# Optimization experiments

Measured on AMD Instinct MI355X. Metric: run time of the kernel, lower is better.

## Reference

```python
import jax, jax.numpy as jnp
import numpy as np
from jax import lax


def _interp_matrix(n_in: int, n_out: int) -> jnp.ndarray:
    """Row-stochastic [n_out, n_in] matrix for 1-D linear interp, align_corners=True."""
    if n_in == 1:
        return jnp.ones((n_out, 1), dtype=jnp.float32)
    pos = jnp.arange(n_out, dtype=jnp.float32) * ((n_in - 1) / (n_out - 1))
    lo = jnp.clip(jnp.floor(pos).astype(jnp.int32), 0, n_in - 2)
    frac = pos - lo.astype(jnp.float32)
    rows = jnp.arange(n_out)
    W = jnp.zeros((n_out, n_in), dtype=jnp.float32)
    W = W.at[rows, lo].add(1.0 - frac)
    W = W.at[rows, lo + 1].add(frac)
    return W


def setup_inputs() -> dict:
    key = jax.random.key(0)
    ks = jax.random.split(key, 10)
    B, C, H, W = 8, 64, 128, 128
    Ch = C // 2
    x = jax.random.normal(ks[0], (B, C, H, W), dtype=jnp.float32)
    # fan-in scaled weights to keep softmax logits in a sane range
    pool_w = jax.random.normal(ks[1], (C, C, 3, 3), dtype=jnp.float32) / np.sqrt(C * 9)
    pool_b = jax.random.normal(ks[2], (C,), dtype=jnp.float32) * 0.1
    q_w = jax.random.normal(ks[3], (Ch, C), dtype=jnp.float32) / np.sqrt(C)
    q_b = jax.random.normal(ks[4], (Ch,), dtype=jnp.float32) * 0.1
    k_w = jax.random.normal(ks[5], (Ch, C), dtype=jnp.float32) / np.sqrt(C)
    k_b = jax.random.normal(ks[6], (Ch,), dtype=jnp.float32) * 0.1
    v_w = jax.random.normal(ks[7], (C, C), dtype=jnp.float32) / np.sqrt(C)
    v_b = jax.random.normal(ks[8], (C,), dtype=jnp.float32) * 0.1
    gamma = jax.random.normal(ks[9], (1,), dtype=jnp.float32)
    return {"x": x, "pool_w": pool_w, "pool_b": pool_b, "q_w": q_w, "q_b": q_b,
            "k_w": k_w, "k_b": k_b, "v_w": v_w, "v_b": v_b, "gamma": gamma}


def reference(x, pool_w, pool_b, q_w, q_b, k_w, k_b, v_w, v_b, gamma):
    # 3x3 stride-2 pad-1 conv (the 'pool')
    xp = lax.conv_general_dilated(x, pool_w, window_strides=(2, 2),
                                  padding=((1, 1), (1, 1)),
                                  dimension_numbers=('NCHW', 'OIHW', 'NCHW'))
    xp = xp + pool_b[None, :, None, None]
    B, C, h, w = xp.shape
    N = h * w
    xf = xp.reshape(B, C, N)  # [B, C, N]
    # 1x1 convs as matmuls over the channel dim
    q = jnp.einsum('oc,bcn->bon', q_w, xf) + q_b[None, :, None]   # [B, C/2, N]
    k = jnp.einsum('oc,bcn->bon', k_w, xf) + k_b[None, :, None]   # [B, C/2, N]
    v = jnp.einsum('oc,bcn->bon', v_w, xf) + v_b[None, :, None]   # [B, C, N]
    # energy[b, n, m] = <q[:, n], k[:, m]>  -> softmax over m
    energy = jnp.einsum('bdn,bdm->bnm', q, k)                     # [B, N, N]
    attn = jax.nn.softmax(energy, axis=-1)
    # out = value @ attention^T  (torch: bmm(v, attn.permute(0,2,1)))
    out = jnp.einsum('bcm,bnm->bcn', v, attn).reshape(B, C, h, w)
    out = gamma[0] * out
    # bilinear upsample to input size, align_corners=True (separable matmuls)
    H, Wd = x.shape[2], x.shape[3]
    Wh = _interp_matrix(h, H)
    Ww = _interp_matrix(w, Wd)
    out = jnp.einsum('Hh,bchw->bcHw', Wh, out)
    out = jnp.einsum('Ww,bchw->bchW', Ww, out)
    return out + x
```

## Files before the change

### kernel.cpp

```cpp
#include <hip/hip_runtime.h>


typedef __attribute__((ext_vector_type(8))) short bf16x8;
typedef __attribute__((ext_vector_type(4))) float f32x4;

#define DEV static __device__ __forceinline__

DEV unsigned f2bf(float f) {
  union { float f; unsigned u; } a; a.f = f;
  return (a.u + 0x7FFFu + ((a.u >> 16) & 1u)) >> 16;
}
DEV unsigned cvtpk(float lo, float hi) {
  unsigned r;
  asm("v_cvt_pk_bf16_f32 %0, %1, %2" : "=v"(r) : "v"(lo), "v"(hi));
  return r;
}
DEV bf16x8 mk_bf16x8(unsigned w0, unsigned w1, unsigned w2, unsigned w3) {
  union { unsigned u[4]; bf16x8 v; } x;
  x.u[0] = w0; x.u[1] = w1; x.u[2] = w2; x.u[3] = w3;
  return x.v;
}
DEV void gload_lds16(const void* g, void* l) {
  __builtin_amdgcn_global_load_lds(
      (const __attribute__((address_space(1))) void*)g,
      (__attribute__((address_space(3))) void*)l, 16, 0, 0);
}

__global__ __launch_bounds__(256) void prep_kernel(
    const float* __restrict__ pw, const float* __restrict__ qw,
    const float* __restrict__ kw, const float* __restrict__ vw,
    const float* __restrict__ qb, const float* __restrict__ kb,
    const float* __restrict__ vb,
    unsigned short* __restrict__ Ag, unsigned short* __restrict__ A2g,
    float* __restrict__ bias2) {
  const float LOG2E = 1.4426950408889634f;
  const int i = blockIdx.x * 256 + threadIdx.x;
  if (i < 36864) {
    const int oc = i / 576, k = i - oc * 576;
    const int tap = k >> 6, ic = k & 63;
    Ag[i] = (unsigned short)f2bf(pw[(oc * 64 + ic) * 9 + tap]);
  }
  const int j = i - 36864;
  if (j >= 0 && j < 8192) {
    const int r = j >> 6, c = j & 63;
    if (r < 32)       A2g[j] = (unsigned short)f2bf(qw[r * 64 + c] * LOG2E);
    else if (r < 64)  A2g[j] = (unsigned short)f2bf(kw[(r - 32) * 64 + c]);
    else              A2g[j] = (unsigned short)f2bf(vw[(r - 64) * 64 + c]);
  }
  if (j >= 8192 && j < 8320) {
    const int r = j - 8192;
    bias2[r] = r < 32 ? qb[r] * LOG2E : (r < 64 ? kb[r - 32] : vb[r - 64]);
  }
}

__global__ __launch_bounds__(256) void convqkv_kernel(
    const float* __restrict__ x, const unsigned short* __restrict__ Ag,
    const float* __restrict__ pool_b, const unsigned short* __restrict__ A2g,
    const float* __restrict__ bias2,
    unsigned short* __restrict__ qT, unsigned short* __restrict__ kT,
    unsigned short* __restrict__ vM) {
  const int b = blockIdx.x >> 6, oy = blockIdx.x & 63;
  const int t = threadIdx.x, w = t >> 6, lane = t & 63;
  const int lr = lane & 15, lg = lane >> 4;
  __shared__ unsigned short sIn[390 * 64];
  __shared__ unsigned short sXP[64 * 64];
  char* sInB = (char*)sIn;
  char* sXPB = (char*)sXP;

  bf16x8 af[18];
  {
    const unsigned short* ap = Ag + (w * 16 + lr) * 576 + (lg << 3);
    #pragma unroll
    for (int kc = 0; kc < 18; ++kc)
      af[kc] = *(const bf16x8*)(ap + kc * 32);
  }

  #pragma unroll
  for (int rr = 0; rr < 2; ++rr) {
    const int pos = t + rr * 256;
    if (pos < 390) {
      const int ky = pos / 130, xi = pos - ky * 130;
      const int iy = 2 * oy + ky - 1, ix = xi - 1;
      const bool ok = (iy >= 0) & (iy < 128) & (ix >= 0) & (ix < 128);
      const float* xs = x + ((size_t)(b * 64) * 128 + (ok ? iy : 0)) * 128 +
                        (ok ? ix : 0);
      const int sw = pos & 7;
      #pragma unroll
      for (int o = 0; o < 8; ++o) {
        float f[8];
        #pragma unroll
        for (int jj = 0; jj < 8; ++jj)
          f[jj] = ok ? xs[(size_t)(o * 8 + jj) * 16384] : 0.f;
        bf16x8 v = mk_bf16x8(cvtpk(f[0], f[1]), cvtpk(f[2], f[3]),
                             cvtpk(f[4], f[5]), cvtpk(f[6], f[7]));
        *(bf16x8*)(sInB + pos * 128 + ((o ^ sw) << 4)) = v;
      }
    }
  }
  __syncthreads();

  f32x4 acc[4];
  #pragma unroll
  for (int nt = 0; nt < 4; ++nt) acc[nt] = (f32x4){0.f, 0.f, 0.f, 0.f};
  #pragma unroll
  for (int kc = 0; kc < 18; ++kc) {
    const int tap = kc >> 1, ky = tap / 3, kx = tap - ky * 3;
    const int o = ((kc & 1) << 2) + lg;
    #pragma unroll
    for (int nt = 0; nt < 4; ++nt) {
      const int xi = 2 * (nt * 16 + lr) + kx;
      const int pos = ky * 130 + xi;
      bf16x8 bfr = *(const bf16x8*)(sInB + pos * 128 + ((o ^ (pos & 7)) << 4));
      acc[nt] = __builtin_amdgcn_mfma_f32_16x16x32_bf16(af[kc], bfr, acc[nt],
                                                        0, 0, 0);
    }
  }

  const int ocBase = w * 16 + (lg << 2);
  float pb[4];
  #pragma unroll
  for (int r = 0; r < 4; ++r) pb[r] = pool_b[ocBase + r];
  const int ocOct = ocBase >> 3;
  const int withinB = (ocBase & 7) * 2;
  #pragma unroll
  for (int nt = 0; nt < 4; ++nt) {
    const int pos = nt * 16 + lr;
    const unsigned p01 = cvtpk(acc[nt][0] + pb[0], acc[nt][1] + pb[1]);
    const unsigned p23 = cvtpk(acc[nt][2] + pb[2], acc[nt][3] + pb[3]);
    char* base = sXPB + pos * 128 + ((ocOct ^ (pos & 7)) << 4) + withinB;
    *(unsigned*)(base) = p01;
    *(unsigned*)(base + 4) = p23;
  }
  __syncthreads();

  bf16x8 a2[2][2];
  #pragma unroll
  for (int mt = 0; mt < 2; ++mt)
    #pragma unroll
    for (int kc2 = 0; kc2 < 2; ++kc2)
      a2[mt][kc2] = *(const bf16x8*)(A2g + ((2 * w + mt) * 16 + lr) * 64 +
                                     kc2 * 32 + (lg << 3));
  f32x4 acc2[2][4];
  #pragma unroll
  for (int mt = 0; mt < 2; ++mt)
    #pragma unroll
    for (int nt = 0; nt < 4; ++nt) acc2[mt][nt] = (f32x4){0.f, 0.f, 0.f, 0.f};
  #pragma unroll
  for (int kc2 = 0; kc2 < 2; ++kc2) {
    const int o2 = (kc2 << 2) + lg;
    #pragma unroll
    for (int nt = 0; nt < 4; ++nt) {
      const int pos = nt * 16 + lr;
      bf16x8 bfr = *(const bf16x8*)(sXPB + pos * 128 + ((o2 ^ (pos & 7)) << 4));
      acc2[0][nt] = __builtin_amdgcn_mfma_f32_16x16x32_bf16(a2[0][kc2], bfr,
                                                            acc2[0][nt], 0, 0, 0);
      acc2[1][nt] = __builtin_amdgcn_mfma_f32_16x16x32_bf16(a2[1][kc2], bfr,
                                                            acc2[1][nt], 0, 0, 0);
    }
  }

  const int n0g = oy << 6;
  #pragma unroll
  for (int mt = 0; mt < 2; ++mt) {
    const int rowB = (2 * w + mt) * 16 + (lg << 2);
    float b2[4];
    #pragma unroll
    for (int r = 0; r < 4; ++r) b2[r] = bias2[rowB + r];
    if (rowB < 32) {
      #pragma unroll
      for (int nt = 0; nt < 4; ++nt) {
        const int n = n0g + nt * 16 + lr;
        unsigned* dst = (unsigned*)(qT + (((size_t)(b << 12) + n) << 5) + rowB);
        dst[0] = cvtpk(acc2[mt][nt][0] + b2[0], acc2[mt][nt][1] + b2[1]);
        dst[1] = cvtpk(acc2[mt][nt][2] + b2[2], acc2[mt][nt][3] + b2[3]);
      }
    } else if (rowB < 64) {
      #pragma unroll
      for (int nt = 0; nt < 4; ++nt) {
        const int n = n0g + nt * 16 + lr;
        unsigned* dst = (unsigned*)(kT + (((size_t)(b << 12) + n) << 5) + rowB - 32);
        dst[0] = cvtpk(acc2[mt][nt][0] + b2[0], acc2[mt][nt][1] + b2[1]);
        dst[1] = cvtpk(acc2[mt][nt][2] + b2[2], acc2[mt][nt][3] + b2[3]);
      }
    } else {
      const int cv = rowB - 64;
      #pragma unroll
      for (int nt = 0; nt < 4; ++nt) {
        const int n = n0g + nt * 16 + lr;
        #pragma unroll
        for (int r = 0; r < 4; ++r)
          vM[(((size_t)(b << 6) + cv + r) << 12) + n] =
              (unsigned short)f2bf(acc2[mt][nt][r] + b2[r]);
      }
    }
  }
}

__global__ __launch_bounds__(256, 2) void attn_kernel(
    const unsigned short* __restrict__ qT, const unsigned short* __restrict__ kT,
    const unsigned short* __restrict__ vM,
    float* __restrict__ attnP, float* __restrict__ Lbuf) {
  __shared__ char lds[24576];
  __shared__ char Plds[4][4608];
  const int t = threadIdx.x, w = t >> 6, lane = t & 63;
  const int lr = lane & 15, lg = lane >> 4;
  const int b = blockIdx.x & 7;
  const int u = (blockIdx.x >> 3) & 31;
  const int split = blockIdx.x >> 8;
  const int n0 = (u << 7) + (w << 5);
  const int kb0 = split << 11;
  char* Pw = Plds[w];

  const unsigned short* qp = qT + (((size_t)(b << 12) + n0 + lr) << 5) + (lg << 3);
  const bf16x8 bq0 = *(const bf16x8*)(qp);
  const bf16x8 bq1 = *(const bf16x8*)(qp + (16 << 5));

  const unsigned short* ksrc = kT + ((size_t)(b << 12) << 5);
  const unsigned short* vsrc = vM + (((size_t)(b << 6) + lane) << 12);

  f32x4 acc[2][4];
  #pragma unroll
  for (int i = 0; i < 2; ++i)
    #pragma unroll
    for (int j = 0; j < 4; ++j) acc[i][j] = (f32x4){0.f, 0.f, 0.f, 0.f};
  float l_run[2] = {0.f, 0.f};

  #define STAGE(kb_, buf_) {                                                   \
    char* sb = lds + (buf_) * 12288;                                           \
    gload_lds16((const void*)(ksrc + (((size_t)(kb_) + lane) << 5) + (w << 3)),\
                sb + (w << 10));                                               \
    gload_lds16((const void*)(vsrc + (kb_) + (w << 4)),                        \
                sb + 4096 + (w << 11));                                        \
    gload_lds16((const void*)(vsrc + (kb_) + (w << 4) + 8),                    \
                sb + 4096 + (w << 11) + 1024);                                 \
  }

  STAGE(kb0, 0);
  __syncthreads();
  int buf = 0;

  for (int cc = 0; cc < 32; ++cc) {
    if (cc < 31) STAGE(kb0 + ((cc + 1) << 6), buf ^ 1);
    char* base = lds + buf * 12288;

    f32x4 st[2][4];
    const f32x4 z4 = {0.f, 0.f, 0.f, 0.f};
    __builtin_amdgcn_s_setprio(1);
    #pragma unroll
    for (int j = 0; j < 4; ++j) {
      const bf16x8 ka =
          *(const bf16x8*)(base + (((lg << 6) + (j << 4) + lr) << 4));
      st[0][j] = __builtin_amdgcn_mfma_f32_16x16x32_bf16(ka, bq0, z4, 0, 0, 0);
      st[1][j] = __builtin_amdgcn_mfma_f32_16x16x32_bf16(ka, bq1, z4, 0, 0, 0);
    }
    __builtin_amdgcn_s_setprio(0);

    #pragma unroll
    for (int nt = 0; nt < 2; ++nt) {
      float ps0 = 0.f, ps1 = 0.f;
      #pragma unroll
      for (int j = 0; j < 4; ++j) {
        const float p0 = __builtin_amdgcn_exp2f(st[nt][j][0]);
        const float p1 = __builtin_amdgcn_exp2f(st[nt][j][1]);
        const float p2 = __builtin_amdgcn_exp2f(st[nt][j][2]);
        const float p3 = __builtin_amdgcn_exp2f(st[nt][j][3]);
        ps0 += p0 + p1;
        ps1 += p2 + p3;
        *(uint2*)(Pw + (nt * 16 + lr) * 144 + (((j << 2) + lg) << 3)) =
            (uint2){cvtpk(p0, p1), cvtpk(p2, p3)};
      }
      l_run[nt] += ps0 + ps1;
    }

    #pragma unroll
    for (int h = 0; h < 2; ++h) {
      #pragma unroll
      for (int nt = 0; nt < 2; ++nt) {
        const bf16x8 pbf = *(const bf16x8*)(
            Pw + (nt * 16 + lr) * 144 + (((h << 3) + (lg << 1)) << 3));
        __builtin_amdgcn_s_setprio(1);
        #pragma unroll
        for (int ct = 0; ct < 4; ++ct) {
          const bf16x8 va = *(const bf16x8*)(
              base + 4096 + (((((h << 2) + lg) << 6) + (ct << 4) + lr) << 4));
          acc[nt][ct] = __builtin_amdgcn_mfma_f32_16x16x32_bf16(va, pbf,
                                                                acc[nt][ct], 0, 0, 0);
        }
        __builtin_amdgcn_s_setprio(0);
      }
    }
    __syncthreads();
    buf ^= 1;
  }

  #pragma unroll
  for (int nt = 0; nt < 2; ++nt) {
    l_run[nt] += __shfl_xor(l_run[nt], 16, 64);
    l_run[nt] += __shfl_xor(l_run[nt], 32, 64);
  }

  float* dstP = attnP + ((size_t)split << 21);
  #pragma unroll
  for (int nt = 0; nt < 2; ++nt) {
    const int q = n0 + (nt << 4) + lr;
    #pragma unroll
    for (int ct = 0; ct < 4; ++ct)
      #pragma unroll
      for (int r = 0; r < 4; ++r) {
        const int c = (ct << 4) + (lg << 2) + r;
        dstP[((size_t)((b << 6) + c) << 12) + q] = acc[nt][ct][r];
      }
  }
  if (lane < 16) {
    Lbuf[((size_t)(split * 8 + b) << 12) + n0 + lane] = l_run[0];
    Lbuf[((size_t)(split * 8 + b) << 12) + n0 + 16 + lane] = l_run[1];
  }
}

__global__ __launch_bounds__(256) void merge_kernel(
    float* __restrict__ attnP, const float* __restrict__ Lbuf,
    const float* __restrict__ gamma_p) {
  const int idx = blockIdx.x * 256 + threadIdx.x;
  const size_t base4 = (size_t)idx << 2;
  const int n4 = (int)(base4 & 4095);
  const int b = (int)(base4 >> 18);
  const f32x4 p0 = *(const f32x4*)(attnP + base4);
  const f32x4 p1 = *(const f32x4*)(attnP + (1u << 21) + base4);
  const f32x4 l0 = *(const f32x4*)(Lbuf + ((size_t)b << 12) + n4);
  const f32x4 l1 = *(const f32x4*)(Lbuf + ((size_t)(8 + b) << 12) + n4);
  const float g = gamma_p[0];
  f32x4 o;
  #pragma unroll
  for (int i = 0; i < 4; ++i) o[i] = (p0[i] + p1[i]) * g / (l0[i] + l1[i]);
  *(f32x4*)(attnP + base4) = o;
}

__global__ __launch_bounds__(256) void upsample_residual_kernel(
    const float* __restrict__ attn_out, const float* __restrict__ x,
    float* __restrict__ out) {
  const int idx = blockIdx.x * 256 + threadIdx.x;
  const int X0 = (idx & 31) << 2;
  int rem = idx >> 5;
  const int Y = rem & 127; rem >>= 7;
  const int c = rem & 63;
  const int b = rem >> 6;

  const float sr = 63.0f / 127.0f;
  float fy = Y * sr;
  int iy = (int)fy; if (iy > 62) iy = 62;
  const float ty = fy - (float)iy;
  const float* ap = attn_out + (((size_t)(b * 64 + c)) << 12);
  const float* r0 = ap + iy * 64;
  const float* r1 = r0 + 64;

  float tmp[4];
  #pragma unroll
  for (int k = 0; k < 4; ++k) {
    const int X = X0 + k;
    float fx = X * sr;
    int ix = (int)fx; if (ix > 62) ix = 62;
    const float tx = fx - (float)ix;
    float v0 = r0[ix] + tx * (r0[ix + 1] - r0[ix]);
    float v1 = r1[ix] + tx * (r1[ix + 1] - r1[ix]);
    tmp[k] = v0 + ty * (v1 - v0);
  }
  const size_t o = (((size_t)((b * 64 + c) * 128 + Y)) << 7) + X0;
  f32x4 xv = *reinterpret_cast<const f32x4*>(x + o);
  f32x4 ov = {tmp[0] + xv[0], tmp[1] + xv[1], tmp[2] + xv[2], tmp[3] + xv[3]};
  *reinterpret_cast<f32x4*>(out + o) = ov;
}

extern "C" void kernel_launch(void* const* d_in, const int* in_sizes, int n_in,
                              void* d_out, int out_size, void* d_ws, size_t ws_size,
                              hipStream_t stream) {
  const float* x      = (const float*)d_in[0];
  const float* pool_w = (const float*)d_in[1];
  const float* pool_b = (const float*)d_in[2];
  const float* q_w    = (const float*)d_in[3];
  const float* q_b    = (const float*)d_in[4];
  const float* k_w    = (const float*)d_in[5];
  const float* k_b    = (const float*)d_in[6];
  const float* v_w    = (const float*)d_in[7];
  const float* v_b    = (const float*)d_in[8];
  const float* gamma  = (const float*)d_in[9];
  float* out = (float*)d_out;

  char* ws = (char*)d_ws;
  unsigned short* Ag   = (unsigned short*)(ws);
  unsigned short* A2g  = (unsigned short*)(ws + 81920);
  float* bias2         = (float*)(ws + 98304);
  unsigned short* qT   = (unsigned short*)(ws + 1048576);
  unsigned short* kT   = (unsigned short*)(ws + 3145728);
  unsigned short* vM   = (unsigned short*)(ws + 5242880);
  float* attnP         = (float*)(ws + 9437184);
  float* Lbuf          = (float*)(ws + 26214400);

  prep_kernel<<<177, 256, 0, stream>>>(pool_w, q_w, k_w, v_w, q_b, k_b, v_b,
                                       Ag, A2g, bias2);
  convqkv_kernel<<<512, 256, 0, stream>>>(x, Ag, pool_b, A2g, bias2, qT, kT, vM);
  attn_kernel<<<512, 256, 0, stream>>>(qT, kT, vM, attnP, Lbuf);
  merge_kernel<<<2048, 256, 0, stream>>>(attnP, Lbuf, gamma);
  upsample_residual_kernel<<<8192, 256, 0, stream>>>(attnP, x, out);
}
```

Before: 93.46 us.

## Halve attention query tile per wave and transpose P via lane shuffles instead of LDS

Each wave now handles 16 queries instead of 32, doubling the grid to 1024 blocks and raising launch_bounds occupancy to 4 blocks per CU. The per-wave P staging buffer in LDS is removed; the exp'd probabilities are repacked into the MFMA B-operand layout with cross-lane shuffles. This aims to cut LDS use and round trips and to raise occupancy so latency is hidden better. In exchange, each K/V tile loaded into LDS is reused by half as many queries, which doubles global K/V traffic.

```diff
diff --git a/kernel.cpp b/kernel.cpp
--- a/kernel.cpp
+++ b/kernel.cpp
@@ -196,34 +196,33 @@
   }
 }
 
-__global__ __launch_bounds__(256, 2) void attn_kernel(
+__global__ __launch_bounds__(256, 4) void attn_kernel(
     const unsigned short* __restrict__ qT, const unsigned short* __restrict__ kT,
     const unsigned short* __restrict__ vM,
     float* __restrict__ attnP, float* __restrict__ Lbuf) {
   __shared__ char lds[24576];
-  __shared__ char Plds[4][4608];
   const int t = threadIdx.x, w = t >> 6, lane = t & 63;
   const int lr = lane & 15, lg = lane >> 4;
   const int b = blockIdx.x & 7;
-  const int u = (blockIdx.x >> 3) & 31;
-  const int split = blockIdx.x >> 8;
-  const int n0 = (u << 7) + (w << 5);
+  const int u = (blockIdx.x >> 3) & 63;
+  const int split = blockIdx.x >> 9;
+  const int n0 = (u << 6) + (w << 4);
   const int kb0 = split << 11;
-  char* Pw = Plds[w];
 
   const unsigned short* qp = qT + (((size_t)(b << 12) + n0 + lr) << 5) + (lg << 3);
-  const bf16x8 bq0 = *(const bf16x8*)(qp);
-  const bf16x8 bq1 = *(const bf16x8*)(qp + (16 << 5));
+  const bf16x8 bq = *(const bf16x8*)(qp);
 
   const unsigned short* ksrc = kT + ((size_t)(b << 12) << 5);
   const unsigned short* vsrc = vM + (((size_t)(b << 6) + lane) << 12);
 
-  f32x4 acc[2][4];
-  #pragma unroll
-  for (int i = 0; i < 2; ++i)
-    #pragma unroll
-    for (int j = 0; j < 4; ++j) acc[i][j] = (f32x4){0.f, 0.f, 0.f, 0.f};
-  float l_run[2] = {0.f, 0.f};
+  f32x4 acc[4];
+  #pragma unroll
+  for (int j = 0; j < 4; ++j) acc[j] = (f32x4){0.f, 0.f, 0.f, 0.f};
+  float l_run = 0.f;
+
+  const int s0 = lr + ((lane & 16) << 1);
+  const int s1 = s0 + 16;
+  const bool hi = (lane & 32) != 0;
 
   #define STAGE(kb_, buf_) {                                                   \
     char* sb = lds + (buf_) * 12288;                                           \
@@ -243,78 +242,75 @@
     if (cc < 31) STAGE(kb0 + ((cc + 1) << 6), buf ^ 1);
     char* base = lds + buf * 12288;
 
-    f32x4 st[2][4];
+    f32x4 st[4];
     const f32x4 z4 = {0.f, 0.f, 0.f, 0.f};
     __builtin_amdgcn_s_setprio(1);
     #pragma unroll
     for (int j = 0; j < 4; ++j) {
       const bf16x8 ka =
           *(const bf16x8*)(base + (((lg << 6) + (j << 4) + lr) << 4));
-      st[0][j] = __builtin_amdgcn_mfma_f32_16x16x32_bf16(ka, bq0, z4, 0, 0, 0);
-      st[1][j] = __builtin_amdgcn_mfma_f32_16x16x32_bf16(ka, bq1, z4, 0, 0, 0);
+      st[j] = __builtin_amdgcn_mfma_f32_16x16x32_bf16(ka, bq, z4, 0, 0, 0);
     }
     __builtin_amdgcn_s_setprio(0);
 
-    #pragma unroll
-    for (int nt = 0; nt < 2; ++nt) {
+    unsigned pw_[4][2];
+    {
       float ps0 = 0.f, ps1 = 0.f;
       #pragma unroll
       for (int j = 0; j < 4; ++j) {
-        const float p0 = __builtin_amdgcn_exp2f(st[nt][j][0]);
-        const float p1 = __builtin_amdgcn_exp2f(st[nt][j][1]);
-        const float p2 = __builtin_amdgcn_exp2f(st[nt][j][2]);
-        const float p3 = __builtin_amdgcn_exp2f(st[nt][j][3]);
+        const float p0 = __builtin_amdgcn_exp2f(st[j][0]);
+        const float p1 = __builtin_amdgcn_exp2f(st[j][1]);
+        const float p2 = __builtin_amdgcn_exp2f(st[j][2]);
+        const float p3 = __builtin_amdgcn_exp2f(st[j][3]);
         ps0 += p0 + p1;
         ps1 += p2 + p3;
-        *(uint2*)(Pw + (nt * 16 + lr) * 144 + (((j << 2) + lg) << 3)) =
-            (uint2){cvtpk(p0, p1), cvtpk(p2, p3)};
-      }
-      l_run[nt] += ps0 + ps1;
+        pw_[j][0] = cvtpk(p0, p1);
+        pw_[j][1] = cvtpk(p2, p3);
+      }
+      l_run += ps0 + ps1;
     }
 
     #pragma unroll
     for (int h = 0; h < 2; ++h) {
-      #pragma unroll
-      for (int nt = 0; nt < 2; ++nt) {
-        const bf16x8 pbf = *(const bf16x8*)(
-            Pw + (nt * 16 + lr) * 144 + (((h << 3) + (lg << 1)) << 3));
-        __builtin_amdgcn_s_setprio(1);
-        #pragma unroll
-        for (int ct = 0; ct < 4; ++ct) {
-          const bf16x8 va = *(const bf16x8*)(
-              base + 4096 + (((((h << 2) + lg) << 6) + (ct << 4) + lr) << 4));
-          acc[nt][ct] = __builtin_amdgcn_mfma_f32_16x16x32_bf16(va, pbf,
-                                                                acc[nt][ct], 0, 0, 0);
-        }
-        __builtin_amdgcn_s_setprio(0);
-      }
+      const int f0 = 2 * h, f1 = 2 * h + 1;
+      const unsigned a0 = __shfl((int)pw_[f0][0], s0, 64);
+      const unsigned a1 = __shfl((int)pw_[f0][1], s0, 64);
+      const unsigned a2 = __shfl((int)pw_[f0][0], s1, 64);
+      const unsigned a3 = __shfl((int)pw_[f0][1], s1, 64);
+      const unsigned c0 = __shfl((int)pw_[f1][0], s0, 64);
+      const unsigned c1 = __shfl((int)pw_[f1][1], s0, 64);
+      const unsigned c2 = __shfl((int)pw_[f1][0], s1, 64);
+      const unsigned c3 = __shfl((int)pw_[f1][1], s1, 64);
+      const bf16x8 pb = hi ? mk_bf16x8(c0, c1, c2, c3)
+                           : mk_bf16x8(a0, a1, a2, a3);
+      __builtin_amdgcn_s_setprio(1);
+      #pragma unroll
+      for (int ct = 0; ct < 4; ++ct) {
+        const bf16x8 va = *(const bf16x8*)(
+            base + 4096 + (((((h << 2) + lg) << 6) + (ct << 4) + lr) << 4));
+        acc[ct] = __builtin_amdgcn_mfma_f32_16x16x32_bf16(va, pb, acc[ct],
+                                                          0, 0, 0);
+      }
+      __builtin_amdgcn_s_setprio(0);
     }
     __syncthreads();
     buf ^= 1;
   }
 
-  #pragma unroll
-  for (int nt = 0; nt < 2; ++nt) {
-    l_run[nt] += __shfl_xor(l_run[nt], 16, 64);
-    l_run[nt] += __shfl_xor(l_run[nt], 32, 64);
-  }
+  l_run += __shfl_xor(l_run, 16, 64);
+  l_run += __shfl_xor(l_run, 32, 64);
 
   float* dstP = attnP + ((size_t)split << 21);
-  #pragma unroll
-  for (int nt = 0; nt < 2; ++nt) {
-    const int q = n0 + (nt << 4) + lr;
-    #pragma unroll
-    for (int ct = 0; ct < 4; ++ct)
-      #pragma unroll
-      for (int r = 0; r < 4; ++r) {
-        const int c = (ct << 4) + (lg << 2) + r;
-        dstP[((size_t)((b << 6) + c) << 12) + q] = acc[nt][ct][r];
-      }
-  }
-  if (lane < 16) {
-    Lbuf[((size_t)(split * 8 + b) << 12) + n0 + lane] = l_run[0];
-    Lbuf[((size_t)(split * 8 + b) << 12) + n0 + 16 + lane] = l_run[1];
-  }
+  const int q = n0 + lr;
+  #pragma unroll
+  for (int ct = 0; ct < 4; ++ct)
+    #pragma unroll
+    for (int r = 0; r < 4; ++r) {
+      const int c = (ct << 4) + (lg << 2) + r;
+      dstP[((size_t)((b << 6) + c) << 12) + q] = acc[ct][r];
+    }
+  if (lane < 16)
+    Lbuf[((size_t)(split * 8 + b) << 12) + n0 + lane] = l_run;
 }
 
 __global__ __launch_bounds__(256) void merge_kernel(
@@ -398,7 +394,7 @@
   prep_kernel<<<177, 256, 0, stream>>>(pool_w, q_w, k_w, v_w, q_b, k_b, v_b,
                                        Ag, A2g, bias2);
   convqkv_kernel<<<512, 256, 0, stream>>>(x, Ag, pool_b, A2g, bias2, qT, kT, vM);
-  attn_kernel<<<512, 256, 0, stream>>>(qT, kT, vM, attnP, Lbuf);
+  attn_kernel<<<1024, 256, 0, stream>>>(qT, kT, vM, attnP, Lbuf);
   merge_kernel<<<2048, 256, 0, stream>>>(attnP, Lbuf, gamma);
   upsample_residual_kernel<<<8192, 256, 0, stream>>>(attnP, x, out);
 }
```

New measurement: 96.16 us. 2.9% more time.

## Restructure attention: 4-way key split, register P exchange, triple-buffered LDS, fused merge

Applied to the files above, without the earlier changes.

Each warp now handles 64 queries, and keys are split four ways instead of two. The K and V tiles are triple-buffered with a swizzled V layout and explicit vmcnt waits. The softmax probabilities move from registers into the MFMA operand layout through lane shuffles instead of an LDS round trip. Partial outputs are stored as bf16, and the separate merge kernel is folded into the upsample kernel, which sums the four partials and the normalisers on the fly. This cuts LDS traffic, global write bandwidth and one launch, at the cost of more registers, extra shuffles, bf16 rounding of the partial sums and redundant merge work per upsampled pixel.

```diff
diff --git a/kernel.cpp b/kernel.cpp
--- a/kernel.cpp
+++ b/kernel.cpp
@@ -9,6 +9,9 @@
 DEV unsigned f2bf(float f) {
   union { float f; unsigned u; } a; a.f = f;
   return (a.u + 0x7FFFu + ((a.u >> 16) & 1u)) >> 16;
+}
+DEV float bf2f(unsigned short v) {
+  union { unsigned u; float f; } a; a.u = ((unsigned)v) << 16; return a.f;
 }
 DEV unsigned cvtpk(float lo, float hi) {
   unsigned r;
@@ -199,64 +202,80 @@
 __global__ __launch_bounds__(256, 2) void attn_kernel(
     const unsigned short* __restrict__ qT, const unsigned short* __restrict__ kT,
     const unsigned short* __restrict__ vM,
-    float* __restrict__ attnP, float* __restrict__ Lbuf) {
-  __shared__ char lds[24576];
-  __shared__ char Plds[4][4608];
+    unsigned short* __restrict__ Pb, float* __restrict__ Lbuf) {
+  __shared__ char lds[36864];
   const int t = threadIdx.x, w = t >> 6, lane = t & 63;
   const int lr = lane & 15, lg = lane >> 4;
   const int b = blockIdx.x & 7;
-  const int u = (blockIdx.x >> 3) & 31;
-  const int split = blockIdx.x >> 8;
-  const int n0 = (u << 7) + (w << 5);
-  const int kb0 = split << 11;
-  char* Pw = Plds[w];
-
-  const unsigned short* qp = qT + (((size_t)(b << 12) + n0 + lr) << 5) + (lg << 3);
-  const bf16x8 bq0 = *(const bf16x8*)(qp);
-  const bf16x8 bq1 = *(const bf16x8*)(qp + (16 << 5));
-
-  const unsigned short* ksrc = kT + ((size_t)(b << 12) << 5);
-  const unsigned short* vsrc = vM + (((size_t)(b << 6) + lane) << 12);
-
-  f32x4 acc[2][4];
-  #pragma unroll
-  for (int i = 0; i < 2; ++i)
-    #pragma unroll
-    for (int j = 0; j < 4; ++j) acc[i][j] = (f32x4){0.f, 0.f, 0.f, 0.f};
-  float l_run[2] = {0.f, 0.f};
-
-  #define STAGE(kb_, buf_) {                                                   \
-    char* sb = lds + (buf_) * 12288;                                           \
-    gload_lds16((const void*)(ksrc + (((size_t)(kb_) + lane) << 5) + (w << 3)),\
-                sb + (w << 10));                                               \
-    gload_lds16((const void*)(vsrc + (kb_) + (w << 4)),                        \
-                sb + 4096 + (w << 11));                                        \
-    gload_lds16((const void*)(vsrc + (kb_) + (w << 4) + 8),                    \
-                sb + 4096 + (w << 11) + 1024);                                 \
-  }
-
-  STAGE(kb0, 0);
-  __syncthreads();
-  int buf = 0;
-
-  for (int cc = 0; cc < 32; ++cc) {
-    if (cc < 31) STAGE(kb0 + ((cc + 1) << 6), buf ^ 1);
-    char* base = lds + buf * 12288;
-
-    f32x4 st[2][4];
+  const int u = (blockIdx.x >> 3) & 15;
+  const int s = blockIdx.x >> 7;
+  const int n0 = (u << 8) + (w << 6);
+  const int kb0 = s << 10;
+
+  bf16x8 bq[4];
+  #pragma unroll
+  for (int nt = 0; nt < 4; ++nt)
+    bq[nt] = *(const bf16x8*)(
+        qT + (((size_t)(b << 12) + n0 + nt * 16 + lr) << 5) + (lg << 3));
+
+  const unsigned short* ksrc = kT + ((size_t)b << 17);
+  const unsigned short* vsrcb = vM + ((size_t)b << 18);
+
+  f32x4 acc[4][4];
+  #pragma unroll
+  for (int nt = 0; nt < 4; ++nt)
+    #pragma unroll
+    for (int ct = 0; ct < 4; ++ct) acc[nt][ct] = (f32x4){0.f, 0.f, 0.f, 0.f};
+  float l_run[4] = {0.f, 0.f, 0.f, 0.f};
+
+  const int s0 = lr + ((lane & 16) << 1);
+  const int s1 = s0 + 16;
+  const bool hi = (lane & 32) != 0;
+  const int vsw = (lane & 7) ^ ((lane >> 3) & 7);
+
+  #define STAGE(ci_) {                                                         \
+    const int kb_ = kb0 + (((ci_) & 15) << 6);                                 \
+    char* sb_ = lds + ((ci_) % 3) * 12288;                                     \
+    gload_lds16((const void*)(ksrc +                                           \
+                  (((size_t)(kb_ + (w << 4) + (lane >> 2))) << 5) +            \
+                  ((lane & 3) << 3)),                                          \
+                sb_ + (w << 10));                                              \
+    gload_lds16((const void*)(vsrcb +                                          \
+                  (((size_t)((w << 4) + (lane >> 3))) << 12) + kb_ +           \
+                  (vsw << 3)),                                                 \
+                sb_ + 4096 + (w << 11));                                       \
+    gload_lds16((const void*)(vsrcb +                                          \
+                  (((size_t)((w << 4) + 8 + (lane >> 3))) << 12) + kb_ +       \
+                  (vsw << 3)),                                                 \
+                sb_ + 4096 + (w << 11) + 1024);                                \
+  }
+
+  STAGE(0);
+  STAGE(1);
+
+  for (int cc = 0; cc < 16; ++cc) {
+    STAGE(cc + 2);
+    asm volatile("s_waitcnt vmcnt(6)" ::: "memory");
+    __builtin_amdgcn_s_barrier();
+    __builtin_amdgcn_sched_barrier(0);
+    char* base = lds + (cc % 3) * 12288;
+
+    f32x4 st[4][4];
     const f32x4 z4 = {0.f, 0.f, 0.f, 0.f};
     __builtin_amdgcn_s_setprio(1);
     #pragma unroll
     for (int j = 0; j < 4; ++j) {
-      const bf16x8 ka =
-          *(const bf16x8*)(base + (((lg << 6) + (j << 4) + lr) << 4));
-      st[0][j] = __builtin_amdgcn_mfma_f32_16x16x32_bf16(ka, bq0, z4, 0, 0, 0);
-      st[1][j] = __builtin_amdgcn_mfma_f32_16x16x32_bf16(ka, bq1, z4, 0, 0, 0);
+      const bf16x8 ka = *(const bf16x8*)(base + ((16 * j + lr) << 6) + (lg << 4));
+      #pragma unroll
+      for (int nt = 0; nt < 4; ++nt)
+        st[nt][j] = __builtin_amdgcn_mfma_f32_16x16x32_bf16(ka, bq[nt], z4,
+                                                            0, 0, 0);
     }
     __builtin_amdgcn_s_setprio(0);
 
-    #pragma unroll
-    for (int nt = 0; nt < 2; ++nt) {
+    unsigned pw_[4][4][2];
+    #pragma unroll
+    for (int nt = 0; nt < 4; ++nt) {
       float ps0 = 0.f, ps1 = 0.f;
       #pragma unroll
       for (int j = 0; j < 4; ++j) {
@@ -266,77 +285,78 @@
         const float p3 = __builtin_amdgcn_exp2f(st[nt][j][3]);
         ps0 += p0 + p1;
         ps1 += p2 + p3;
-        *(uint2*)(Pw + (nt * 16 + lr) * 144 + (((j << 2) + lg) << 3)) =
-            (uint2){cvtpk(p0, p1), cvtpk(p2, p3)};
+        pw_[nt][j][0] = cvtpk(p0, p1);
+        pw_[nt][j][1] = cvtpk(p2, p3);
       }
       l_run[nt] += ps0 + ps1;
     }
 
     #pragma unroll
     for (int h = 0; h < 2; ++h) {
-      #pragma unroll
-      for (int nt = 0; nt < 2; ++nt) {
-        const bf16x8 pbf = *(const bf16x8*)(
-            Pw + (nt * 16 + lr) * 144 + (((h << 3) + (lg << 1)) << 3));
-        __builtin_amdgcn_s_setprio(1);
+      bf16x8 pbv[4];
+      #pragma unroll
+      for (int nt = 0; nt < 4; ++nt) {
+        const int f0 = 2 * h, f1 = 2 * h + 1;
+        const unsigned a0 = __shfl((int)pw_[nt][f0][0], s0, 64);
+        const unsigned a1 = __shfl((int)pw_[nt][f0][1], s0, 64);
+        const unsigned a2 = __shfl((int)pw_[nt][f0][0], s1, 64);
+        const unsigned a3 = __shfl((int)pw_[nt][f0][1], s1, 64);
+        const unsigned c0 = __shfl((int)pw_[nt][f1][0], s0, 64);
+        const unsigned c1 = __shfl((int)pw_[nt][f1][1], s0, 64);
+        const unsigned c2 = __shfl((int)pw_[nt][f1][0], s1, 64);
+        const unsigned c3 = __shfl((int)pw_[nt][f1][1], s1, 64);
+        pbv[nt] = hi ? mk_bf16x8(c0, c1, c2, c3) : mk_bf16x8(a0, a1, a2, a3);
+      }
+      __builtin_amdgcn_s_setprio(1);
+      #pragma unroll
+      for (int ct = 0; ct < 4; ++ct) {
+        const int c = (ct << 4) + lr;
+        const int o = (h << 2) + lg;
+        const bf16x8 va = *(const bf16x8*)(
+            base + 4096 + (c << 7) + ((o ^ (lr & 7)) << 4));
         #pragma unroll
-        for (int ct = 0; ct < 4; ++ct) {
-          const bf16x8 va = *(const bf16x8*)(
-              base + 4096 + (((((h << 2) + lg) << 6) + (ct << 4) + lr) << 4));
-          acc[nt][ct] = __builtin_amdgcn_mfma_f32_16x16x32_bf16(va, pbf,
-                                                                acc[nt][ct], 0, 0, 0);
-        }
-        __builtin_amdgcn_s_setprio(0);
-      }
-    }
-    __syncthreads();
-    buf ^= 1;
-  }
-
-  #pragma unroll
-  for (int nt = 0; nt < 2; ++nt) {
+        for (int nt = 0; nt < 4; ++nt)
+          acc[nt][ct] = __builtin_amdgcn_mfma_f32_16x16x32_bf16(va, pbv[nt],
+                                                                acc[nt][ct],
+                                                                0, 0, 0);
+      }
+      __builtin_amdgcn_s_setprio(0);
+    }
+
+    __builtin_amdgcn_sched_barrier(0);
+    asm volatile("s_waitcnt lgkmcnt(0)" ::: "memory");
+    __builtin_amdgcn_s_barrier();
+  }
+
+  #pragma unroll
+  for (int nt = 0; nt < 4; ++nt) {
     l_run[nt] += __shfl_xor(l_run[nt], 16, 64);
     l_run[nt] += __shfl_xor(l_run[nt], 32, 64);
   }
 
-  float* dstP = attnP + ((size_t)split << 21);
-  #pragma unroll
-  for (int nt = 0; nt < 2; ++nt) {
-    const int q = n0 + (nt << 4) + lr;
+  unsigned short* dst = Pb + ((size_t)s << 21);
+  #pragma unroll
+  for (int nt = 0; nt < 4; ++nt) {
+    const int q = n0 + nt * 16 + lr;
     #pragma unroll
     for (int ct = 0; ct < 4; ++ct)
       #pragma unroll
       for (int r = 0; r < 4; ++r) {
         const int c = (ct << 4) + (lg << 2) + r;
-        dstP[((size_t)((b << 6) + c) << 12) + q] = acc[nt][ct][r];
+        dst[((size_t)((b << 6) + c) << 12) + q] =
+            (unsigned short)f2bf(acc[nt][ct][r]);
       }
   }
   if (lane < 16) {
-    Lbuf[((size_t)(split * 8 + b) << 12) + n0 + lane] = l_run[0];
-    Lbuf[((size_t)(split * 8 + b) << 12) + n0 + 16 + lane] = l_run[1];
-  }
-}
-
-__global__ __launch_bounds__(256) void merge_kernel(
-    float* __restrict__ attnP, const float* __restrict__ Lbuf,
-    const float* __restrict__ gamma_p) {
-  const int idx = blockIdx.x * 256 + threadIdx.x;
-  const size_t base4 = (size_t)idx << 2;
-  const int n4 = (int)(base4 & 4095);
-  const int b = (int)(base4 >> 18);
-  const f32x4 p0 = *(const f32x4*)(attnP + base4);
-  const f32x4 p1 = *(const f32x4*)(attnP + (1u << 21) + base4);
-  const f32x4 l0 = *(const f32x4*)(Lbuf + ((size_t)b << 12) + n4);
-  const f32x4 l1 = *(const f32x4*)(Lbuf + ((size_t)(8 + b) << 12) + n4);
-  const float g = gamma_p[0];
-  f32x4 o;
-  #pragma unroll
-  for (int i = 0; i < 4; ++i) o[i] = (p0[i] + p1[i]) * g / (l0[i] + l1[i]);
-  *(f32x4*)(attnP + base4) = o;
+    #pragma unroll
+    for (int nt = 0; nt < 4; ++nt)
+      Lbuf[((size_t)(s * 8 + b) << 12) + n0 + nt * 16 + lane] = l_run[nt];
+  }
 }
 
 __global__ __launch_bounds__(256) void upsample_residual_kernel(
-    const float* __restrict__ attn_out, const float* __restrict__ x,
+    const unsigned short* __restrict__ Pb, const float* __restrict__ Lbuf,
+    const float* __restrict__ gamma_p, const float* __restrict__ x,
     float* __restrict__ out) {
   const int idx = blockIdx.x * 256 + threadIdx.x;
   const int X0 = (idx & 31) << 2;
@@ -344,24 +364,41 @@
   const int Y = rem & 127; rem >>= 7;
   const int c = rem & 63;
   const int b = rem >> 6;
+  const float g = gamma_p[0];
 
   const float sr = 63.0f / 127.0f;
-  float fy = Y * sr;
+  const float fy = Y * sr;
   int iy = (int)fy; if (iy > 62) iy = 62;
   const float ty = fy - (float)iy;
-  const float* ap = attn_out + (((size_t)(b * 64 + c)) << 12);
-  const float* r0 = ap + iy * 64;
-  const float* r1 = r0 + 64;
+
+  const unsigned short* prow = Pb + (((size_t)((b << 6) + c)) << 12);
+  const float* lrow = Lbuf + ((size_t)b << 12);
+  const int ix0 = (int)(X0 * sr);
+
+  float a[2][4];
+  #pragma unroll
+  for (int rr = 0; rr < 2; ++rr)
+    #pragma unroll
+    for (int jj = 0; jj < 4; ++jj) {
+      int col = ix0 + jj; if (col > 63) col = 63;
+      const int n = (iy + rr) * 64 + col;
+      const float num = bf2f(prow[n]) + bf2f(prow[(1u << 21) + n]) +
+                        bf2f(prow[(2u << 21) + n]) + bf2f(prow[(3u << 21) + n]);
+      const float den = lrow[n] + lrow[32768 + n] + lrow[65536 + n] +
+                        lrow[98304 + n];
+      a[rr][jj] = g * num / den;
+    }
 
   float tmp[4];
   #pragma unroll
   for (int k = 0; k < 4; ++k) {
     const int X = X0 + k;
-    float fx = X * sr;
+    const float fx = X * sr;
     int ix = (int)fx; if (ix > 62) ix = 62;
     const float tx = fx - (float)ix;
-    float v0 = r0[ix] + tx * (r0[ix + 1] - r0[ix]);
-    float v1 = r1[ix] + tx * (r1[ix + 1] - r1[ix]);
+    const int li = ix - ix0;
+    const float v0 = a[0][li] + tx * (a[0][li + 1] - a[0][li]);
+    const float v1 = a[1][li] + tx * (a[1][li + 1] - a[1][li]);
     tmp[k] = v0 + ty * (v1 - v0);
   }
   const size_t o = (((size_t)((b * 64 + c) * 128 + Y)) << 7) + X0;
@@ -392,13 +429,12 @@
   unsigned short* qT   = (unsigned short*)(ws + 1048576);
   unsigned short* kT   = (unsigned short*)(ws + 3145728);
   unsigned short* vM   = (unsigned short*)(ws + 5242880);
-  float* attnP         = (float*)(ws + 9437184);
+  unsigned short* Pb   = (unsigned short*)(ws + 9437184);
   float* Lbuf          = (float*)(ws + 26214400);
 
   prep_kernel<<<177, 256, 0, stream>>>(pool_w, q_w, k_w, v_w, q_b, k_b, v_b,
                                        Ag, A2g, bias2);
   convqkv_kernel<<<512, 256, 0, stream>>>(x, Ag, pool_b, A2g, bias2, qT, kT, vM);
-  attn_kernel<<<512, 256, 0, stream>>>(qT, kT, vM, attnP, Lbuf);
-  merge_kernel<<<2048, 256, 0, stream>>>(attnP, Lbuf, gamma);
-  upsample_residual_kernel<<<8192, 256, 0, stream>>>(attnP, x, out);
-}
+  attn_kernel<<<512, 256, 0, stream>>>(qT, kT, vM, Pb, Lbuf);
+  upsample_residual_kernel<<<8192, 256, 0, stream>>>(Pb, Lbuf, gamma, x, out);
+}
```

Result: slower. 136.4 us (+45.9%).
